# Optimization experiments

Hardware: AMD Instinct MI355X
Metric: run time of the kernel (lower is better)

The kernel has to match this reference:

```python
import jax, jax.numpy as jnp
import numpy as np

B, N, C = 8, 1024, 768
H = 12
HD = C // H
FF = 2048
NUM_CLASSES = 1000
SCALE = HD ** -0.5


def layer_norm(x, g, b, eps=1e-5):
    mu = jnp.mean(x, axis=-1, keepdims=True)
    var = jnp.var(x, axis=-1, keepdims=True)
    return (x - mu) * jax.lax.rsqrt(var + eps) * g + b


def setup_inputs() -> dict:
    key = jax.random.key(0)
    ks = jax.random.split(key, 12)
    s = lambda *sh: 0.02
    return {
        "src": jax.random.normal(ks[0], (B, N, C), jnp.float32),
        "y": jax.random.uniform(ks[1], (B, NUM_CLASSES), jnp.float32),
        "scorenet_h_src": jax.random.normal(ks[2], (B, NUM_CLASSES), jnp.float32),
        "pre_g": jnp.ones((C,), jnp.float32),
        "pre_b": jnp.zeros((C,), jnp.float32),
        "qkv_w": jax.random.normal(ks[3], (C, 3 * C), jnp.float32) * 0.02,
        "proj_w": jax.random.normal(ks[4], (C, C), jnp.float32) * 0.02,
        "proj_b": jnp.zeros((C,), jnp.float32),
        "n1_g": jnp.ones((C,), jnp.float32),
        "n1_b": jnp.zeros((C,), jnp.float32),
        "l1_w": jax.random.normal(ks[5], (C, FF), jnp.float32) * 0.02,
        "l1_b": jnp.zeros((FF,), jnp.float32),
        "l2_w": jax.random.normal(ks[6], (FF, C), jnp.float32) * 0.02,
        "l2_b": jnp.zeros((C,), jnp.float32),
    }


def attention(x, qkv_w, proj_w, proj_b):
    # x: [B, N, C] -> qkv: [B, N, 3, H, HD]
    qkv = (x @ qkv_w).reshape(B, N, 3, H, HD)
    qkv = jnp.transpose(qkv, (2, 0, 3, 1, 4))  # [3, B, H, N, HD]
    q, k, v = qkv[0], qkv[1], qkv[2]
    attn = jax.nn.softmax(jnp.einsum("bhqd,bhkd->bhqk", q, k) * SCALE, axis=-1)
    out = jnp.einsum("bhqk,bhkd->bhqd", attn, v)  # [B, H, N, HD]
    out = jnp.transpose(out, (0, 2, 1, 3)).reshape(B, N, C)
    out = out @ proj_w + proj_b
    return out, attn


def reference(src, y, scorenet_h_src, pre_g, pre_b, qkv_w, proj_w, proj_b,
              n1_g, n1_b, l1_w, l1_b, l2_w, l2_b):
    # eval-mode forward: dropout / drop_path are identity, mixup branches off
    x, attn = attention(layer_norm(src, pre_g, pre_b), qkv_w, proj_w, proj_b)
    src = src + x
    src_n = layer_norm(src, n1_g, n1_b)
    ffn = jax.nn.gelu(src_n @ l1_w + l1_b, approximate=False) @ l2_w + l2_b
    src = src_n + ffn
    return (src, scorenet_h_src, y, attn)
```

## Files before the change

kernel.cpp:

```cpp
#include <hip/hip_runtime.h>
#include <stdint.h>

typedef unsigned short u16;
typedef __bf16 bf16x8 __attribute__((ext_vector_type(8)));
typedef float f32x4 __attribute__((ext_vector_type(4)));


__device__ __forceinline__ u16 f2bf(float f) {
  union { float f; unsigned u; } v; v.f = f;
  unsigned r = v.u + 0x7fffu + ((v.u >> 16) & 1u);
  return (u16)(r >> 16);
}
__device__ __forceinline__ float bf2f(unsigned u) {
  union { unsigned u; float f; } v; v.u = u << 16; return v.f;
}

__device__ __forceinline__ void async16(const void* g, void* l) {
  __builtin_amdgcn_global_load_lds(
      (const __attribute__((address_space(1))) void*)g,
      (__attribute__((address_space(3))) void*)l, 16, 0, 0);
}

__device__ __forceinline__ f32x4 mfma16(bf16x8 a, bf16x8 b, f32x4 c) {
  return __builtin_amdgcn_mfma_f32_16x16x32_bf16(a, b, c, 0, 0, 0);
}

__device__ __forceinline__ float gelu_exact(float x) {
  return 0.5f * x * (1.0f + erff(x * 0.70710678118654752440f));
}

__global__ __launch_bounds__(256) void ln_kernel(
    const float* __restrict__ x, const float* __restrict__ g,
    const float* __restrict__ b, u16* __restrict__ obf,
    float* __restrict__ of) {
  const size_t row = blockIdx.x;
  const float* xr = x + row * 768;
  const int t = threadIdx.x;
  const int w = t >> 6, lane = t & 63;
  float v0 = xr[t], v1 = xr[t + 256], v2 = xr[t + 512];
  float s = v0 + v1 + v2;
  float sq = v0 * v0 + v1 * v1 + v2 * v2;
#pragma unroll
  for (int off = 32; off > 0; off >>= 1) {
    s += __shfl_down(s, off);
    sq += __shfl_down(sq, off);
  }
  __shared__ float ss[4], ssq[4];
  if (lane == 0) { ss[w] = s; ssq[w] = sq; }
  __syncthreads();
  s = ss[0] + ss[1] + ss[2] + ss[3];
  sq = ssq[0] + ssq[1] + ssq[2] + ssq[3];
  const float mean = s * (1.0f / 768.0f);
  const float var = sq * (1.0f / 768.0f) - mean * mean;
  const float rstd = rsqrtf(var + 1e-5f);
  float y0 = (v0 - mean) * rstd * g[t] + b[t];
  float y1 = (v1 - mean) * rstd * g[t + 256] + b[t + 256];
  float y2 = (v2 - mean) * rstd * g[t + 512] + b[t + 512];
  obf[row * 768 + t] = f2bf(y0);
  obf[row * 768 + t + 256] = f2bf(y1);
  obf[row * 768 + t + 512] = f2bf(y2);
  if (of) {
    of[row * 768 + t] = y0;
    of[row * 768 + t + 256] = y1;
    of[row * 768 + t + 512] = y2;
  }
}

__device__ __forceinline__ void transpose_tile(float (*tile)[33],
                                               const float* __restrict__ W,
                                               u16* __restrict__ Wt, int K,
                                               int N, int bx, int by) {
  const int n0 = bx * 32, k0 = by * 32;
  const int tx = threadIdx.x, ty = threadIdx.y;
  for (int r = ty; r < 32; r += 8)
    tile[r][tx] = W[(size_t)(k0 + r) * N + n0 + tx];
  __syncthreads();
  for (int r = ty; r < 32; r += 8)
    Wt[(size_t)(n0 + r) * K + k0 + tx] = f2bf(tile[tx][r]);
}

__global__ void misc_kernel(const float* __restrict__ qkv_w,
                            const float* __restrict__ proj_w,
                            const float* __restrict__ l1_w,
                            const float* __restrict__ l2_w,
                            u16* __restrict__ qkvwT, u16* __restrict__ projwT,
                            u16* __restrict__ l1wT, u16* __restrict__ l2wT,
                            const float* __restrict__ y,
                            const float* __restrict__ sc,
                            float* __restrict__ out) {
  __shared__ float tile[32][33];
  int bid = blockIdx.x;
  if (bid < 1728) { transpose_tile(tile, qkv_w, qkvwT, 768, 2304, bid % 72, bid / 72); return; }
  bid -= 1728;
  if (bid < 576) { transpose_tile(tile, proj_w, projwT, 768, 768, bid % 24, bid / 24); return; }
  bid -= 576;
  if (bid < 1536) { transpose_tile(tile, l1_w, l1wT, 768, 2048, bid % 64, bid / 64); return; }
  bid -= 1536;
  if (bid < 1536) { transpose_tile(tile, l2_w, l2wT, 2048, 768, bid % 24, bid / 24); return; }
  bid -= 1536;
  const int t = threadIdx.y * 32 + threadIdx.x;
  const int i = bid * 256 + t;
  if (i < 8000) {
    out[6291456 + i] = sc[i];
    out[6299456 + i] = y[i];
  }
}

__global__ void vt_kernel(const u16* __restrict__ qkv, u16* __restrict__ vt) {
  const int bh = blockIdx.z, b = bh / 12, h = bh % 12;
  const int n0 = blockIdx.x * 32, d0 = blockIdx.y * 32;
  __shared__ u16 tile[32][33];
  const u16* Vp = qkv + (size_t)b * 1024 * 2304 + 1536 + h * 64;
  const int tx = threadIdx.x, ty = threadIdx.y;
  for (int r = ty; r < 32; r += 8)
    tile[r][tx] = Vp[(size_t)(n0 + r) * 2304 + d0 + tx];
  __syncthreads();
  u16* Op = vt + (size_t)bh * 64 * 1024;
  for (int r = ty; r < 32; r += 8)
    Op[(size_t)(d0 + r) * 1024 + n0 + tx] = tile[tx][r];
}

template <int BM, int BN, int GN, int WM, int WN>
__global__ __launch_bounds__(256) void gemm_kernel(
    const u16* __restrict__ A, int lda, const u16* __restrict__ Bt, int ldb,
    const float* __restrict__ bias, const float* __restrict__ res,
    float* __restrict__ outF, u16* __restrict__ outB, int ldc, int K,
    int act) {
  __shared__ u16 As[BM * 32];
  __shared__ u16 Bs[BN * 32];
  const int tid = threadIdx.x;
  const int w = tid >> 6, lane = tid & 63;
  const size_t mBase = (size_t)blockIdx.y * BM;
  const size_t nBase = (size_t)blockIdx.x * BN;
  const int rq = lane >> 2;
  const int k8 = (lane & 3) * 8;
  const int wmBase = (w / GN) * (WM * 16);
  const int wnBase = (w % GN) * (WN * 16);
  const int tm = lane & 15, kq = lane >> 4;
  const f32x4 zero = {0.f, 0.f, 0.f, 0.f};
  f32x4 acc[WM][WN];
#pragma unroll
  for (int i = 0; i < WM; i++)
#pragma unroll
    for (int j = 0; j < WN; j++) acc[i][j] = zero;

  for (int kt = 0; kt < K; kt += 32) {
    __syncthreads();
#pragma unroll
    for (int c = w; c < BM / 16; c += 4)
      async16(A + (mBase + c * 16 + rq) * lda + kt + k8, &As[c * 16 * 32]);
#pragma unroll
    for (int c = w; c < BN / 16; c += 4)
      async16(Bt + (nBase + c * 16 + rq) * ldb + kt + k8, &Bs[c * 16 * 32]);
    __syncthreads();
    bf16x8 af[WM], bfv[WN];
#pragma unroll
    for (int i = 0; i < WM; i++)
      af[i] = *(const bf16x8*)&As[(wmBase + i * 16 + tm) * 32 + kq * 8];
#pragma unroll
    for (int j = 0; j < WN; j++)
      bfv[j] = *(const bf16x8*)&Bs[(wnBase + j * 16 + tm) * 32 + kq * 8];
#pragma unroll
    for (int i = 0; i < WM; i++)
#pragma unroll
      for (int j = 0; j < WN; j++) acc[i][j] = mfma16(af[i], bfv[j], acc[i][j]);
  }

#pragma unroll
  for (int i = 0; i < WM; i++) {
    const size_t row0 = mBase + wmBase + i * 16 + kq * 4;
#pragma unroll
    for (int j = 0; j < WN; j++) {
      const size_t col = nBase + wnBase + j * 16 + tm;
      const float bv = bias ? bias[col] : 0.0f;
#pragma unroll
      for (int r = 0; r < 4; r++) {
        const size_t rr = row0 + r;
        float v = acc[i][j][r] + bv;
        if (act) v = gelu_exact(v);
        if (res) v += res[rr * ldc + col];
        if (outF) outF[rr * ldc + col] = v;
        if (outB) outB[rr * ldc + col] = f2bf(v);
      }
    }
  }
}

__global__ __launch_bounds__(256) void flash_kernel(
    const u16* __restrict__ qkv, const u16* __restrict__ vt,
    float* __restrict__ attn, u16* __restrict__ aout) {
  __shared__ u16 Pt[16][1032];
  __shared__ u16 Ks[128][68];
  __shared__ u16 Qs[16][68];
  __shared__ u16 Vs[64][66];
  __shared__ float rinv[16];
  const int tid = threadIdx.x;
  const int w = tid >> 6, lane = tid & 63;
  const int tm = lane & 15, kq = lane >> 4;
  const int bh = blockIdx.y, b = bh / 12, h = bh % 12;
  const size_t m0 = (size_t)blockIdx.x * 16;
  const u16* Qp = qkv + (size_t)b * 1024 * 2304 + h * 64;
  const u16* Kp = Qp + 768;
  const u16* Vp = vt + (size_t)bh * 64 * 1024;
  float* Ab = attn + (size_t)bh * 1024 * 1024 + m0 * 1024;

  if (tid < 128) {
    const int r = tid >> 3, kc = tid & 7;
    *(uint4*)&Qs[r][kc * 8] = *(const uint4*)(Qp + (m0 + r) * 2304 + kc * 8);
  }

  for (int nc = 0; nc < 1024; nc += 128) {
    __syncthreads();
#pragma unroll
    for (int u = 0; u < 4; ++u) {
      const int idx = u * 256 + tid;
      const int r = idx >> 3, kc = idx & 7;
      *(uint4*)&Ks[r][kc * 8] =
          *(const uint4*)(Kp + (size_t)(nc + r) * 2304 + kc * 8);
    }
    __syncthreads();
    const bf16x8 aq0 = *(const bf16x8*)&Qs[tm][kq * 8];
    const bf16x8 aq1 = *(const bf16x8*)&Qs[tm][32 + kq * 8];
    const int n0 = w * 32;
    const bf16x8 b00 = *(const bf16x8*)&Ks[n0 + tm][kq * 8];
    const bf16x8 b01 = *(const bf16x8*)&Ks[n0 + tm][32 + kq * 8];
    const bf16x8 b10 = *(const bf16x8*)&Ks[n0 + 16 + tm][kq * 8];
    const bf16x8 b11 = *(const bf16x8*)&Ks[n0 + 16 + tm][32 + kq * 8];
    f32x4 acc0 = {0.f, 0.f, 0.f, 0.f}, acc1 = {0.f, 0.f, 0.f, 0.f};
    acc0 = mfma16(aq0, b00, acc0);
    acc0 = mfma16(aq1, b01, acc0);
    acc1 = mfma16(aq0, b10, acc1);
    acc1 = mfma16(aq1, b11, acc1);
#pragma unroll
    for (int r = 0; r < 4; ++r) {
      const int row = kq * 4 + r;
      Pt[row][nc + n0 + tm] = f2bf(__expf(acc0[r] * 0.125f));
      Pt[row][nc + n0 + 16 + tm] = f2bf(__expf(acc1[r] * 0.125f));
    }
  }
  __syncthreads();

#pragma unroll
  for (int rr = 0; rr < 4; ++rr) {
    const int row = w * 4 + rr;
    float s = 0.f;
#pragma unroll
    for (int c = 0; c < 4; ++c) {
      const uint2 pk = *(const uint2*)&Pt[row][(c * 64 + lane) * 4];
      s += bf2f(pk.x & 0xffffu) + bf2f(pk.x >> 16) + bf2f(pk.y & 0xffffu) +
           bf2f(pk.y >> 16);
    }
#pragma unroll
    for (int off = 32; off > 0; off >>= 1) s += __shfl_xor(s, off);
    if (lane == 0) rinv[row] = 1.0f / s;
  }
  __syncthreads();

#pragma unroll
  for (int rr = 0; rr < 4; ++rr) {
    const int row = w * 4 + rr;
    const float inv = rinv[row];
#pragma unroll
    for (int c = 0; c < 4; ++c) {
      const int col = (c * 64 + lane) * 4;
      const uint2 pk = *(const uint2*)&Pt[row][col];
      float4 o;
      o.x = bf2f(pk.x & 0xffffu) * inv;
      o.y = bf2f(pk.x >> 16) * inv;
      o.z = bf2f(pk.y & 0xffffu) * inv;
      o.w = bf2f(pk.y >> 16) * inv;
      *(float4*)&Ab[(size_t)row * 1024 + col] = o;
    }
  }

  f32x4 oacc = {0.f, 0.f, 0.f, 0.f};
  for (int kt = 0; kt < 1024; kt += 64) {
    __syncthreads();
    {
      const int d = tid >> 2, kc = (tid & 3) * 8;
      *(uint4*)&Vs[d][kc] = *(const uint4*)(Vp + (size_t)d * 1024 + kt + kc);
      *(uint4*)&Vs[d][32 + kc] =
          *(const uint4*)(Vp + (size_t)d * 1024 + kt + 32 + kc);
    }
    __syncthreads();
    const bf16x8 ap0 = *(const bf16x8*)&Pt[tm][kt + kq * 8];
    const bf16x8 ap1 = *(const bf16x8*)&Pt[tm][kt + 32 + kq * 8];
    const bf16x8 bv0 = *(const bf16x8*)&Vs[w * 16 + tm][kq * 8];
    const bf16x8 bv1 = *(const bf16x8*)&Vs[w * 16 + tm][32 + kq * 8];
    oacc = mfma16(ap0, bv0, oacc);
    oacc = mfma16(ap1, bv1, oacc);
  }

  const size_t orow0 = (size_t)b * 1024 + m0;
#pragma unroll
  for (int r = 0; r < 4; ++r) {
    const int m = kq * 4 + r;
    aout[(orow0 + m) * 768 + h * 64 + w * 16 + tm] = f2bf(oacc[r] * rinv[m]);
  }
}

extern "C" void kernel_launch(void* const* d_in, const int* in_sizes, int n_in,
                              void* d_out, int out_size, void* d_ws,
                              size_t ws_size, hipStream_t stream) {
  const float* src    = (const float*)d_in[0];
  const float* yin    = (const float*)d_in[1];
  const float* scin   = (const float*)d_in[2];
  const float* pre_g  = (const float*)d_in[3];
  const float* pre_b  = (const float*)d_in[4];
  const float* qkv_w  = (const float*)d_in[5];
  const float* proj_w = (const float*)d_in[6];
  const float* proj_b = (const float*)d_in[7];
  const float* n1_g   = (const float*)d_in[8];
  const float* n1_b   = (const float*)d_in[9];
  const float* l1_w   = (const float*)d_in[10];
  const float* l1_b   = (const float*)d_in[11];
  const float* l2_w   = (const float*)d_in[12];
  const float* l2_b   = (const float*)d_in[13];
  float* outp = (float*)d_out;
  float* attn = outp + 6307456;

  char* ws = (char*)d_ws;
  u16* qkvwT  = (u16*)(ws + 0ull);
  u16* projwT = (u16*)(ws + 3538944ull);
  u16* l1wT   = (u16*)(ws + 4718592ull);
  u16* l2wT   = (u16*)(ws + 7864320ull);
  const size_t P0 = 11010048ull;
  u16* xn   = (u16*)(ws + P0);
  u16* qkv  = (u16*)(ws + P0 + 12582912ull);
  u16* vt   = (u16*)(ws + P0 + 50331648ull);
  u16* aout = (u16*)(ws + P0 + 62914560ull);
  float* src2 = (float*)(ws + P0);
  u16*  snb   = (u16*)(ws + P0 + 25165824ull);
  u16*  hbuf  = (u16*)(ws + P0 + 37748736ull);
  float* snf  = (float*)(ws + P0 + 71303168ull);

  dim3 tb(32, 8);
  misc_kernel<<<5439, tb, 0, stream>>>(qkv_w, proj_w, l1_w, l2_w, qkvwT,
                                       projwT, l1wT, l2wT, yin, scin, outp);
  ln_kernel<<<8192, 256, 0, stream>>>(src, pre_g, pre_b, xn, nullptr);
  gemm_kernel<128, 128, 2, 4, 4><<<dim3(18, 64), 256, 0, stream>>>(
      xn, 768, qkvwT, 768, nullptr, nullptr, nullptr, qkv, 2304, 768, 0);
  vt_kernel<<<dim3(32, 2, 96), tb, 0, stream>>>(qkv, vt);
  flash_kernel<<<dim3(64, 96), 256, 0, stream>>>(qkv, vt, attn, aout);
  gemm_kernel<64, 128, 4, 4, 2><<<dim3(6, 128), 256, 0, stream>>>(
      aout, 768, projwT, 768, proj_b, src, src2, nullptr, 768, 768, 0);
  ln_kernel<<<8192, 256, 0, stream>>>(src2, n1_g, n1_b, snb, snf);
  gemm_kernel<128, 128, 2, 4, 4><<<dim3(16, 64), 256, 0, stream>>>(
      snb, 768, l1wT, 768, l1_b, nullptr, nullptr, hbuf, 2048, 768, 1);
  gemm_kernel<64, 128, 4, 4, 2><<<dim3(6, 128), 256, 0, stream>>>(
      hbuf, 2048, l2wT, 2048, l2_b, snf, outp, nullptr, 768, 2048, 0);
}
```

Before: 935.7 us.

## Restructure attention kernel into two-pass softmax with 32-row tiles and swizzled LDS

```diff
diff --git a/kernel.cpp b/kernel.cpp
--- a/kernel.cpp
+++ b/kernel.cpp
@@ -186,117 +186,151 @@
   }
 }
 
-__global__ __launch_bounds__(256) void flash_kernel(
+__global__ __launch_bounds__(256, 3) void flash_kernel(
     const u16* __restrict__ qkv, const u16* __restrict__ vt,
     float* __restrict__ attn, u16* __restrict__ aout) {
-  __shared__ u16 Pt[16][1032];
-  __shared__ u16 Ks[128][68];
-  __shared__ u16 Qs[16][68];
-  __shared__ u16 Vs[64][66];
-  __shared__ float rinv[16];
+  __shared__ u16 Qs[32 * 64];
+  __shared__ u16 KV[2 * 128 * 64];
+  __shared__ u16 Ps[32 * 128];
+  __shared__ float psum[4][32];
+  __shared__ float rinv[32];
   const int tid = threadIdx.x;
   const int w = tid >> 6, lane = tid & 63;
   const int tm = lane & 15, kq = lane >> 4;
   const int bh = blockIdx.y, b = bh / 12, h = bh % 12;
-  const size_t m0 = (size_t)blockIdx.x * 16;
+  const size_t m0 = (size_t)blockIdx.x * 32;
   const u16* Qp = qkv + (size_t)b * 1024 * 2304 + h * 64;
   const u16* Kp = Qp + 768;
   const u16* Vp = vt + (size_t)bh * 64 * 1024;
-  float* Ab = attn + (size_t)bh * 1024 * 1024 + m0 * 1024;
-
-  if (tid < 128) {
-    const int r = tid >> 3, kc = tid & 7;
-    *(uint4*)&Qs[r][kc * 8] = *(const uint4*)(Qp + (m0 + r) * 2304 + kc * 8);
-  }
-
-  for (int nc = 0; nc < 1024; nc += 128) {
+  float* Ab = attn + ((size_t)bh * 1024 + m0) * 1024;
+
+  {
+    const int r = tid >> 3, c = tid & 7;
+    *(uint4*)&Qs[r * 64 + ((c ^ (r & 7)) * 8)] =
+        *(const uint4*)(Qp + (m0 + r) * 2304 + c * 8);
+  }
+  __syncthreads();
+  bf16x8 aq[2][2];
+#pragma unroll
+  for (int i = 0; i < 2; i++)
+#pragma unroll
+    for (int k2 = 0; k2 < 2; k2++) {
+      const int m = i * 16 + tm;
+      aq[i][k2] =
+          *(const bf16x8*)&Qs[m * 64 + (((k2 * 4 + kq) ^ (m & 7)) * 8)];
+    }
+
+  f32x4 rs[2] = {{0.f, 0.f, 0.f, 0.f}, {0.f, 0.f, 0.f, 0.f}};
+  for (int cc = 0; cc < 4; ++cc) {
+    const int nc = cc * 256;
+    __syncthreads();
+#pragma unroll
+    for (int u = 0; u < 8; ++u) {
+      const int idx = u * 256 + tid;
+      const int r = idx >> 3, c = idx & 7;
+      *(uint4*)&KV[r * 64 + ((c ^ (r & 7)) * 8)] =
+          *(const uint4*)(Kp + (size_t)(nc + r) * 2304 + c * 8);
+    }
+    __syncthreads();
+#pragma unroll
+    for (int jj = 0; jj < 4; ++jj) {
+      const int n = (w * 4 + jj) * 16 + tm;
+      bf16x8 bk[2];
+#pragma unroll
+      for (int k2 = 0; k2 < 2; k2++)
+        bk[k2] =
+            *(const bf16x8*)&KV[n * 64 + (((k2 * 4 + kq) ^ (n & 7)) * 8)];
+#pragma unroll
+      for (int i = 0; i < 2; i++) {
+        f32x4 s = {0.f, 0.f, 0.f, 0.f};
+        s = mfma16(aq[i][0], bk[0], s);
+        s = mfma16(aq[i][1], bk[1], s);
+#pragma unroll
+        for (int r = 0; r < 4; r++) rs[i][r] += __expf(s[r] * 0.125f);
+      }
+    }
+  }
+#pragma unroll
+  for (int i = 0; i < 2; i++)
+#pragma unroll
+    for (int r = 0; r < 4; r++) {
+      float v = rs[i][r];
+      v += __shfl_xor(v, 1); v += __shfl_xor(v, 2);
+      v += __shfl_xor(v, 4); v += __shfl_xor(v, 8);
+      if (tm == 0) psum[w][i * 16 + kq * 4 + r] = v;
+    }
+  __syncthreads();
+  if (tid < 32)
+    rinv[tid] =
+        1.0f / (psum[0][tid] + psum[1][tid] + psum[2][tid] + psum[3][tid]);
+
+  const f32x4 zero = {0.f, 0.f, 0.f, 0.f};
+  f32x4 oacc[2] = {zero, zero};
+  const int mi = w & 1, dp = w >> 1;
+  for (int cc = 0; cc < 8; ++cc) {
+    const int nc = cc * 128;
     __syncthreads();
 #pragma unroll
     for (int u = 0; u < 4; ++u) {
       const int idx = u * 256 + tid;
-      const int r = idx >> 3, kc = idx & 7;
-      *(uint4*)&Ks[r][kc * 8] =
-          *(const uint4*)(Kp + (size_t)(nc + r) * 2304 + kc * 8);
-    }
-    __syncthreads();
-    const bf16x8 aq0 = *(const bf16x8*)&Qs[tm][kq * 8];
-    const bf16x8 aq1 = *(const bf16x8*)&Qs[tm][32 + kq * 8];
-    const int n0 = w * 32;
-    const bf16x8 b00 = *(const bf16x8*)&Ks[n0 + tm][kq * 8];
-    const bf16x8 b01 = *(const bf16x8*)&Ks[n0 + tm][32 + kq * 8];
-    const bf16x8 b10 = *(const bf16x8*)&Ks[n0 + 16 + tm][kq * 8];
-    const bf16x8 b11 = *(const bf16x8*)&Ks[n0 + 16 + tm][32 + kq * 8];
-    f32x4 acc0 = {0.f, 0.f, 0.f, 0.f}, acc1 = {0.f, 0.f, 0.f, 0.f};
-    acc0 = mfma16(aq0, b00, acc0);
-    acc0 = mfma16(aq1, b01, acc0);
-    acc1 = mfma16(aq0, b10, acc1);
-    acc1 = mfma16(aq1, b11, acc1);
+      const int r = idx >> 3, c = idx & 7;
+      *(uint4*)&KV[r * 64 + ((c ^ (r & 7)) * 8)] =
+          *(const uint4*)(Kp + (size_t)(nc + r) * 2304 + c * 8);
+    }
+#pragma unroll
+    for (int u = 0; u < 4; ++u) {
+      const int idx = u * 256 + tid;
+      const int d = idx >> 4, c = idx & 15;
+      *(uint4*)&KV[8192 + d * 128 + ((c ^ (d & 15)) * 8)] =
+          *(const uint4*)(Vp + (size_t)d * 1024 + nc + c * 8);
+    }
+    __syncthreads();
+#pragma unroll
+    for (int jj = 0; jj < 2; ++jj) {
+      const int nb = w * 2 + jj;
+      const int n = nb * 16 + tm;
+      bf16x8 bk[2];
+#pragma unroll
+      for (int k2 = 0; k2 < 2; k2++)
+        bk[k2] =
+            *(const bf16x8*)&KV[n * 64 + (((k2 * 4 + kq) ^ (n & 7)) * 8)];
+#pragma unroll
+      for (int i = 0; i < 2; i++) {
+        f32x4 s = {0.f, 0.f, 0.f, 0.f};
+        s = mfma16(aq[i][0], bk[0], s);
+        s = mfma16(aq[i][1], bk[1], s);
+        const int row = i * 16 + kq * 4;
+#pragma unroll
+        for (int r = 0; r < 4; r++) {
+          const float p = __expf(s[r] * 0.125f) * rinv[row + r];
+          Ab[(size_t)(row + r) * 1024 + nc + nb * 16 + tm] = p;
+          const int pr = row + r, pn = nb * 16 + tm;
+          Ps[pr * 128 + (((pn >> 3) ^ (pr & 7)) * 8) + (pn & 7)] = f2bf(p);
+        }
+      }
+    }
+    __syncthreads();
+#pragma unroll
+    for (int k2 = 0; k2 < 4; ++k2) {
+      const int m = mi * 16 + tm;
+      const bf16x8 ap =
+          *(const bf16x8*)&Ps[m * 128 + (((k2 * 4 + kq) ^ (m & 7)) * 8)];
+#pragma unroll
+      for (int jd = 0; jd < 2; ++jd) {
+        const int d = dp * 32 + jd * 16 + tm;
+        const bf16x8 bv = *(const bf16x8*)&KV[8192 + d * 128 +
+                                              (((k2 * 4 + kq) ^ (d & 15)) * 8)];
+        oacc[jd] = mfma16(ap, bv, oacc[jd]);
+      }
+    }
+  }
+#pragma unroll
+  for (int jd = 0; jd < 2; ++jd)
 #pragma unroll
     for (int r = 0; r < 4; ++r) {
-      const int row = kq * 4 + r;
-      Pt[row][nc + n0 + tm] = f2bf(__expf(acc0[r] * 0.125f));
-      Pt[row][nc + n0 + 16 + tm] = f2bf(__expf(acc1[r] * 0.125f));
-    }
-  }
-  __syncthreads();
-
-#pragma unroll
-  for (int rr = 0; rr < 4; ++rr) {
-    const int row = w * 4 + rr;
-    float s = 0.f;
-#pragma unroll
-    for (int c = 0; c < 4; ++c) {
-      const uint2 pk = *(const uint2*)&Pt[row][(c * 64 + lane) * 4];
-      s += bf2f(pk.x & 0xffffu) + bf2f(pk.x >> 16) + bf2f(pk.y & 0xffffu) +
-           bf2f(pk.y >> 16);
-    }
-#pragma unroll
-    for (int off = 32; off > 0; off >>= 1) s += __shfl_xor(s, off);
-    if (lane == 0) rinv[row] = 1.0f / s;
-  }
-  __syncthreads();
-
-#pragma unroll
-  for (int rr = 0; rr < 4; ++rr) {
-    const int row = w * 4 + rr;
-    const float inv = rinv[row];
-#pragma unroll
-    for (int c = 0; c < 4; ++c) {
-      const int col = (c * 64 + lane) * 4;
-      const uint2 pk = *(const uint2*)&Pt[row][col];
-      float4 o;
-      o.x = bf2f(pk.x & 0xffffu) * inv;
-      o.y = bf2f(pk.x >> 16) * inv;
-      o.z = bf2f(pk.y & 0xffffu) * inv;
-      o.w = bf2f(pk.y >> 16) * inv;
-      *(float4*)&Ab[(size_t)row * 1024 + col] = o;
-    }
-  }
-
-  f32x4 oacc = {0.f, 0.f, 0.f, 0.f};
-  for (int kt = 0; kt < 1024; kt += 64) {
-    __syncthreads();
-    {
-      const int d = tid >> 2, kc = (tid & 3) * 8;
-      *(uint4*)&Vs[d][kc] = *(const uint4*)(Vp + (size_t)d * 1024 + kt + kc);
-      *(uint4*)&Vs[d][32 + kc] =
-          *(const uint4*)(Vp + (size_t)d * 1024 + kt + 32 + kc);
-    }
-    __syncthreads();
-    const bf16x8 ap0 = *(const bf16x8*)&Pt[tm][kt + kq * 8];
-    const bf16x8 ap1 = *(const bf16x8*)&Pt[tm][kt + 32 + kq * 8];
-    const bf16x8 bv0 = *(const bf16x8*)&Vs[w * 16 + tm][kq * 8];
-    const bf16x8 bv1 = *(const bf16x8*)&Vs[w * 16 + tm][32 + kq * 8];
-    oacc = mfma16(ap0, bv0, oacc);
-    oacc = mfma16(ap1, bv1, oacc);
-  }
-
-  const size_t orow0 = (size_t)b * 1024 + m0;
-#pragma unroll
-  for (int r = 0; r < 4; ++r) {
-    const int m = kq * 4 + r;
-    aout[(orow0 + m) * 768 + h * 64 + w * 16 + tm] = f2bf(oacc[r] * rinv[m]);
-  }
+      const size_t gm = (size_t)b * 1024 + m0 + mi * 16 + kq * 4 + r;
+      aout[gm * 768 + h * 64 + dp * 32 + jd * 16 + tm] = f2bf(oacc[jd][r]);
+    }
 }
 
 extern "C" void kernel_launch(void* const* d_in, const int* in_sizes, int n_in,
@@ -341,7 +375,7 @@
   gemm_kernel<128, 128, 2, 4, 4><<<dim3(18, 64), 256, 0, stream>>>(
       xn, 768, qkvwT, 768, nullptr, nullptr, nullptr, qkv, 2304, 768, 0);
   vt_kernel<<<dim3(32, 2, 96), tb, 0, stream>>>(qkv, vt);
-  flash_kernel<<<dim3(64, 96), 256, 0, stream>>>(qkv, vt, attn, aout);
+  flash_kernel<<<dim3(32, 96), 256, 0, stream>>>(qkv, vt, attn, aout);
   gemm_kernel<64, 128, 4, 4, 2><<<dim3(6, 128), 256, 0, stream>>>(
       aout, 768, projwT, 768, proj_b, src, src2, nullptr, 768, 768, 0);
   ln_kernel<<<8192, 256, 0, stream>>>(src2, n1_g, n1_b, snb, snf);
```

New measurement: 819.4 us. -12.4%, faster.
